# Kernel optimization log

Measured on AMD Instinct MI355X. Metric: run time of the kernel, lower is better.

## Reference

```python
import jax, jax.numpy as jnp
import numpy as np

N = 40000; E = 640000; F_IN = 128; HID = 32; HEADS = 4; G = 64
NEG_SLOPE = 0.2; LN_EPS = 1e-5


def setup_inputs() -> dict:
    key = jax.random.key(0)
    ks = jax.random.split(key, 24)
    rn = lambda k, shape, s=0.1: jax.random.normal(k, shape, jnp.float32) * s
    d = {}
    d["x"] = jax.random.normal(ks[0], (N, F_IN), jnp.float32)
    d["edge_index"] = jax.random.randint(ks[1], (2, E), 0, N)
    d["batch"] = jnp.sort(jax.random.randint(ks[2], (N,), 0, G))
    # GAT layer 0: in F_IN -> HID per head, HEADS heads, concat
    d["W0"] = rn(ks[3], (F_IN, HEADS * HID))
    d["as0"] = rn(ks[4], (HEADS, HID)); d["ad0"] = rn(ks[5], (HEADS, HID))
    d["b0"] = jnp.zeros((HEADS * HID,), jnp.float32)
    d["ln0_g"] = jnp.ones((HEADS * HID,), jnp.float32); d["ln0_b"] = jnp.zeros((HEADS * HID,), jnp.float32)
    # GAT layer 1: HEADS*HID -> HID per head, HEADS heads, concat
    d["W1"] = rn(ks[6], (HEADS * HID, HEADS * HID))
    d["as1"] = rn(ks[7], (HEADS, HID)); d["ad1"] = rn(ks[8], (HEADS, HID))
    d["b1"] = jnp.zeros((HEADS * HID,), jnp.float32)
    d["ln1_g"] = jnp.ones((HEADS * HID,), jnp.float32); d["ln1_b"] = jnp.zeros((HEADS * HID,), jnp.float32)
    # GAT layer 2: HEADS*HID -> HID, 1 head, no concat
    d["W2"] = rn(ks[9], (HEADS * HID, HID))
    d["as2"] = rn(ks[10], (1, HID)); d["ad2"] = rn(ks[11], (1, HID))
    d["b2"] = jnp.zeros((HID,), jnp.float32)
    d["ln2_g"] = jnp.ones((HID,), jnp.float32); d["ln2_b"] = jnp.zeros((HID,), jnp.float32)
    # classifier: HID -> HID//2 -> 2
    d["fc1_w"] = rn(ks[12], (HID, HID // 2)); d["fc1_b"] = jnp.zeros((HID // 2,), jnp.float32)
    d["fc2_w"] = rn(ks[13], (HID // 2, 2)); d["fc2_b"] = jnp.zeros((2,), jnp.float32)
    return d


def gat_layer(x, src, dst, W, a_s, a_d, b, heads, out_c, concat):
    n = x.shape[0]
    h = (x @ W).reshape(n, heads, out_c)            # [N,H,C]
    al_s = jnp.sum(h * a_s, axis=-1)                # [N,H]
    al_d = jnp.sum(h * a_d, axis=-1)                # [N,H]
    e = jax.nn.leaky_relu(al_s[src] + al_d[dst], NEG_SLOPE)  # [E,H]
    m = jax.ops.segment_max(e, dst, num_segments=n)          # segment softmax over dst
    ex = jnp.exp(e - m[dst])
    s = jax.ops.segment_sum(ex, dst, num_segments=n)
    alpha = ex / (s[dst] + 1e-16)                   # [E,H]
    out = jax.ops.segment_sum(h[src] * alpha[:, :, None], dst, num_segments=n)  # [N,H,C]
    out = out.reshape(n, heads * out_c) if concat else out.mean(axis=1)
    return out + b


def layer_norm(x, g, b):
    mu = x.mean(-1, keepdims=True)
    var = jnp.var(x, axis=-1, keepdims=True)
    return (x - mu) * jax.lax.rsqrt(var + LN_EPS) * g + b


def reference(x, edge_index, batch, W0, as0, ad0, b0, ln0_g, ln0_b, W1, as1, ad1, b1, ln1_g, ln1_b, W2, as2, ad2, b2, ln2_g, ln2_b, fc1_w, fc1_b, fc2_w, fc2_b):
    src, dst = edge_index[0], edge_index[1]
    h = gat_layer(x, src, dst, W0, as0, ad0, b0, HEADS, HID, True)
    h = jax.nn.elu(layer_norm(h, ln0_g, ln0_b))
    h = gat_layer(h, src, dst, W1, as1, ad1, b1, HEADS, HID, True)
    h = jax.nn.elu(layer_norm(h, ln1_g, ln1_b))
    h = gat_layer(h, src, dst, W2, as2, ad2, b2, 1, HID, False)
    h = jax.nn.elu(layer_norm(h, ln2_g, ln2_b))
    cnt = jax.ops.segment_sum(jnp.ones((h.shape[0],), h.dtype), batch, num_segments=G)
    hg = jax.ops.segment_sum(h, batch, num_segments=G) / jnp.maximum(cnt, 1.0)[:, None]  # global mean pool [G,HID]
    z = jax.nn.relu(hg @ fc1_w + fc1_b)
    return z @ fc2_w + fc2_b
```

## Files before the change

### kernel.cpp

```cpp
#include <hip/hip_runtime.h>
#include <hip/hip_fp16.h>
#include <math.h>

#define NN 40000
#define EE 640000
#define NG 64
#define SCAN_BLOCKS ((NN + 1023) / 1024)

__device__ __forceinline__ float eluf(float x) { return x > 0.f ? x : expm1f(x); }

typedef const __attribute__((address_space(1))) char gas_char;
typedef __attribute__((address_space(3))) char las_char;

__device__ __forceinline__ void async_copy16(void* l, const void* g) {
  __builtin_amdgcn_global_load_lds((gas_char*)g, (las_char*)l, 16, 0, 0);
}

typedef __fp16 f16x2 __attribute__((ext_vector_type(2)));
__device__ __forceinline__ unsigned packh(float lo, float hi) {
  f16x2 p = __builtin_amdgcn_cvt_pkrtz(lo, hi);
  union { f16x2 h; unsigned u; } c; c.h = p; return c.u;
}
__device__ __forceinline__ float hlo(unsigned p) {
  union { unsigned u; f16x2 h; } c; c.u = p; return (float)c.h.x;
}
__device__ __forceinline__ float hhi(unsigned p) {
  union { unsigned u; f16x2 h; } c; c.u = p; return (float)c.h.y;
}

__global__ void zero_int_kernel(int* __restrict__ p, int n) {
  int i = blockIdx.x * 256 + threadIdx.x;
  if (i < n) p[i] = 0;
}

__global__ void count_deg_kernel(const int* __restrict__ dst, int* __restrict__ deg, int e) {
  int i0 = (blockIdx.x * 256 + threadIdx.x) * 2;
  if (i0 + 2 <= e) {
    int2 d2 = *reinterpret_cast<const int2*>(&dst[i0]);
    atomicAdd(&deg[d2.x], 1);
    atomicAdd(&deg[d2.y], 1);
  } else {
    for (int i = i0; i < e; ++i) atomicAdd(&deg[dst[i]], 1);
  }
}

__global__ __launch_bounds__(1024) void scanA_kernel(const int* __restrict__ deg,
                                                     int* __restrict__ row_ptr,
                                                     int* __restrict__ bsum, int n) {
  __shared__ int wsum[16];
  int t = threadIdx.x, lane = t & 63, wid = t >> 6;
  int i = blockIdx.x * 1024 + t;
  int v = (i < n) ? deg[i] : 0;
#pragma unroll
  for (int off = 1; off < 64; off <<= 1) {
    int u = __shfl_up(v, off);
    if (lane >= off) v += u;
  }
  if (lane == 63) wsum[wid] = v;
  __syncthreads();
  if (t < 16) {
    int w = wsum[t];
#pragma unroll
    for (int off = 1; off < 16; off <<= 1) {
      int u = __shfl_up(w, off);
      if (t >= off) w += u;
    }
    wsum[t] = w;
  }
  __syncthreads();
  if (wid > 0) v += wsum[wid - 1];
  if (i < n) row_ptr[i + 1] = v;
  if (t == 1023) bsum[blockIdx.x] = v;
}

__global__ __launch_bounds__(1024) void scanC_kernel(int* __restrict__ row_ptr,
                                                     const int* __restrict__ bsum,
                                                     int* __restrict__ cursor, int n) {
  __shared__ int off_s;
  int t = threadIdx.x;
  int b = blockIdx.x;
  if (t < 64) {
    int v = (t < b && t < SCAN_BLOCKS) ? bsum[t] : 0;
#pragma unroll
    for (int m = 1; m < 64; m <<= 1) v += __shfl_xor(v, m);
    if (t == 0) off_s = v;
  }
  __syncthreads();
  int off = off_s;
  int i = b * 1024 + t;
  if (i < n) {
    int v = row_ptr[i + 1] + off;
    row_ptr[i + 1] = v;
    if (i + 1 < n) cursor[i + 1] = v;
    if (i == 0) { cursor[0] = 0; row_ptr[0] = 0; }
  }
}

__global__ void scatter_kernel(const int* __restrict__ src, const int* __restrict__ dst,
                               int* __restrict__ cursor, int* __restrict__ csr_src, int e) {
  int i0 = (blockIdx.x * 256 + threadIdx.x) * 2;
  if (i0 + 2 <= e) {
    int2 s2 = *reinterpret_cast<const int2*>(&src[i0]);
    int2 d2 = *reinterpret_cast<const int2*>(&dst[i0]);
    int p0 = atomicAdd(&cursor[d2.x], 1);
    int p1 = atomicAdd(&cursor[d2.y], 1);
    csr_src[p0] = s2.x;
    csr_src[p1] = s2.y;
  } else {
    for (int i = i0; i < e; ++i) {
      int d = dst[i];
      int pos = atomicAdd(&cursor[d], 1);
      csr_src[pos] = src[i];
    }
  }
}

__global__ __launch_bounds__(256, 3) void gemm128_kernel(
    const float* __restrict__ x, const float* __restrict__ W,
    const float* __restrict__ a_s, const float* __restrict__ a_d,
    unsigned* __restrict__ hb, float* __restrict__ als, float* __restrict__ ald)
{
  __shared__ float xs[2][64 * 32];
  __shared__ float ws[2][32 * 128];

  int t = threadIdx.x;
  int row0 = blockIdx.x * 64;
  const char* xgb = (const char*)x + (size_t)row0 * 512;

  {
    int li0 = t, li1 = t + 256;
    async_copy16((char*)xs[0] + li0 * 16, xgb + (li0 >> 3) * 512 + (li0 & 7) * 16);
    async_copy16((char*)xs[0] + li1 * 16, xgb + (li1 >> 3) * 512 + (li1 & 7) * 16);
    const char* wg = (const char*)W;
#pragma unroll
    for (int p = 0; p < 4; ++p)
      async_copy16((char*)ws[0] + p * 4096 + t * 16, wg + p * 4096 + t * 16);
  }
  __syncthreads();

  int cg = t & 31, rg = t >> 5;
  int r0 = rg * 8;
  int jlo = 2 * cg;

  float acc[8][4];
#pragma unroll
  for (int r = 0; r < 8; ++r)
#pragma unroll
    for (int c = 0; c < 4; ++c) acc[r][c] = 0.f;

  for (int ch = 0; ch < 4; ++ch) {
    if (ch < 3) {
      int b = (ch + 1) & 1;
      int li0 = t, li1 = t + 256;
      const char* xg = xgb + (ch + 1) * 128;
      async_copy16((char*)xs[b] + li0 * 16, xg + (li0 >> 3) * 512 + (li0 & 7) * 16);
      async_copy16((char*)xs[b] + li1 * 16, xg + (li1 >> 3) * 512 + (li1 & 7) * 16);
      const char* wg = (const char*)W + (size_t)(ch + 1) * 32 * 128 * 4;
#pragma unroll
      for (int p = 0; p < 4; ++p)
        async_copy16((char*)ws[b] + p * 4096 + t * 16, wg + p * 4096 + t * 16);
    }
    const float* wc = ws[ch & 1];
    const float* xc = xs[ch & 1];
#pragma unroll
    for (int kk = 0; kk < 32; kk += 4) {
      float2 wlo[4], whi[4];
#pragma unroll
      for (int q = 0; q < 4; ++q) {
        wlo[q] = *reinterpret_cast<const float2*>(&wc[(kk + q) * 128 + jlo]);
        whi[q] = *reinterpret_cast<const float2*>(&wc[(kk + q) * 128 + 64 + jlo]);
      }
#pragma unroll
      for (int r = 0; r < 8; ++r) {
        float4 xv = *reinterpret_cast<const float4*>(&xc[(r0 + r) * 32 + kk]);
        float a0 = acc[r][0], a1 = acc[r][1], a2 = acc[r][2], a3 = acc[r][3];
        a0 = fmaf(xv.x, wlo[0].x, a0); a1 = fmaf(xv.x, wlo[0].y, a1);
        a2 = fmaf(xv.x, whi[0].x, a2); a3 = fmaf(xv.x, whi[0].y, a3);
        a0 = fmaf(xv.y, wlo[1].x, a0); a1 = fmaf(xv.y, wlo[1].y, a1);
        a2 = fmaf(xv.y, whi[1].x, a2); a3 = fmaf(xv.y, whi[1].y, a3);
        a0 = fmaf(xv.z, wlo[2].x, a0); a1 = fmaf(xv.z, wlo[2].y, a1);
        a2 = fmaf(xv.z, whi[2].x, a2); a3 = fmaf(xv.z, whi[2].y, a3);
        a0 = fmaf(xv.w, wlo[3].x, a0); a1 = fmaf(xv.w, wlo[3].y, a1);
        a2 = fmaf(xv.w, whi[3].x, a2); a3 = fmaf(xv.w, whi[3].y, a3);
        acc[r][0] = a0; acc[r][1] = a1; acc[r][2] = a2; acc[r][3] = a3;
      }
    }
    __syncthreads();
  }

#pragma unroll
  for (int r = 0; r < 8; ++r) {
    uint2 pv;
    pv.x = packh(acc[r][0], acc[r][2]);
    pv.y = packh(acc[r][1], acc[r][3]);
    *reinterpret_cast<uint2*>(&hb[(size_t)(row0 + r0 + r) * 64 + jlo]) = pv;
  }

  float as0 = a_s[jlo], as1 = a_s[jlo + 1], as2 = a_s[jlo + 64], as3 = a_s[jlo + 65];
  float ad0 = a_d[jlo], ad1 = a_d[jlo + 1], ad2 = a_d[jlo + 64], ad3 = a_d[jlo + 65];
  int lane = t & 63;
#pragma unroll
  for (int r = 0; r < 8; ++r) {
    float psa = fmaf(acc[r][0], as0, acc[r][1] * as1);
    float psb = fmaf(acc[r][2], as2, acc[r][3] * as3);
    float pda = fmaf(acc[r][0], ad0, acc[r][1] * ad1);
    float pdb = fmaf(acc[r][2], ad2, acc[r][3] * ad3);
#pragma unroll
    for (int m = 1; m < 16; m <<= 1) {
      psa += __shfl_xor(psa, m); psb += __shfl_xor(psb, m);
      pda += __shfl_xor(pda, m); pdb += __shfl_xor(pdb, m);
    }
    if ((lane & 15) == 0) {
      int hA = (lane >> 4) & 1;
      size_t row = (size_t)(row0 + r0 + r);
      als[row * 4 + hA] = psa; als[row * 4 + hA + 2] = psb;
      ald[row * 4 + hA] = pda; ald[row * 4 + hA + 2] = pdb;
    }
  }
}

template<bool FUSE>
__global__ __launch_bounds__(256) void aggregate128_kernel(
    const unsigned* __restrict__ hb, const float* __restrict__ als, const float* __restrict__ ald,
    const int* __restrict__ row_ptr, const int* __restrict__ csr_src,
    const float* __restrict__ bias, const float* __restrict__ ln_g, const float* __restrict__ ln_b,
    float* __restrict__ out,
    const float* __restrict__ W2, const float* __restrict__ as2, const float* __restrict__ ad2,
    unsigned short* __restrict__ h2h, float* __restrict__ als2, float* __restrict__ ald2)
{
  __shared__ int s_src[4][4][17];
  __shared__ float2 s_w[4][4][17][2];
  __shared__ __align__(16) float w2s[FUSE ? 32 * 128 : 4];
  __shared__ __align__(16) float y_s[FUSE ? 16 * 132 : 4];

  int t = threadIdx.x, lane = t & 63, wid = t >> 6;
  int q = lane >> 4, c4 = lane & 15;
  int node = blockIdx.x * 16 + wid * 4 + q;

  if constexpr (FUSE) {
#pragma unroll
    for (int p = 0; p < 4; ++p)
      async_copy16((char*)w2s + p * 4096 + t * 16, (const char*)W2 + p * 4096 + t * 16);
    __syncthreads();
  }

  int start = row_ptr[node], end = row_ptr[node + 1];
  int deg = end - start;

  float4 adq = reinterpret_cast<const float4*>(ald)[node];
  int hsel = c4 >> 3;
  const uint4* hbase = reinterpret_cast<const uint4*>(hb + 4 * c4);
  float a0 = 0.f, a1 = 0.f, a2 = 0.f, a3 = 0.f;
  float a4 = 0.f, a5 = 0.f, a6 = 0.f, a7 = 0.f;
  float b0 = 0.f, b1 = 0.f, b2 = 0.f, b3 = 0.f;
  float b4 = 0.f, b5 = 0.f, b6 = 0.f, b7 = 0.f;
  float ssum0 = 0.f, ssum1 = 0.f, sb0 = 0.f, sb1 = 0.f;

  for (int eb = 0; eb < deg; eb += 16) {
    int s = 0;
    float ex0 = 0.f, ex1 = 0.f, ex2 = 0.f, ex3 = 0.f;
    if (eb + c4 < deg) {
      s = csr_src[start + eb + c4];
      float4 qv = reinterpret_cast<const float4*>(als)[s];
      float v0 = qv.x + adq.x, v1 = qv.y + adq.y, v2 = qv.z + adq.z, v3 = qv.w + adq.w;
      v0 = v0 > 0.f ? v0 : 0.2f * v0; v1 = v1 > 0.f ? v1 : 0.2f * v1;
      v2 = v2 > 0.f ? v2 : 0.2f * v2; v3 = v3 > 0.f ? v3 : 0.2f * v3;
      ex0 = __expf(v0); ex1 = __expf(v1); ex2 = __expf(v2); ex3 = __expf(v3);
    }
    s_src[wid][q][c4] = s;
    s_w[wid][q][c4][0] = make_float2(ex0, ex2);
    s_w[wid][q][c4][1] = make_float2(ex1, ex3);

    int cnt = deg - eb; if (cnt > 16) cnt = 16;
    int j = 0;
    for (; j + 2 <= cnt; j += 2) {
      int sa = s_src[wid][q][j];
      int sb = s_src[wid][q][j + 1];
      uint4 ua = hbase[(size_t)sa * 16];
      uint4 ub = hbase[(size_t)sb * 16];
      float2 wa = s_w[wid][q][j][hsel];
      float2 wb = s_w[wid][q][j + 1][hsel];
      a0 = fmaf(wa.x, hlo(ua.x), a0); a1 = fmaf(wa.x, hlo(ua.y), a1);
      a2 = fmaf(wa.x, hlo(ua.z), a2); a3 = fmaf(wa.x, hlo(ua.w), a3);
      a4 = fmaf(wa.y, hhi(ua.x), a4); a5 = fmaf(wa.y, hhi(ua.y), a5);
      a6 = fmaf(wa.y, hhi(ua.z), a6); a7 = fmaf(wa.y, hhi(ua.w), a7);
      ssum0 += wa.x; ssum1 += wa.y;
      b0 = fmaf(wb.x, hlo(ub.x), b0); b1 = fmaf(wb.x, hlo(ub.y), b1);
      b2 = fmaf(wb.x, hlo(ub.z), b2); b3 = fmaf(wb.x, hlo(ub.w), b3);
      b4 = fmaf(wb.y, hhi(ub.x), b4); b5 = fmaf(wb.y, hhi(ub.y), b5);
      b6 = fmaf(wb.y, hhi(ub.z), b6); b7 = fmaf(wb.y, hhi(ub.w), b7);
      sb0 += wb.x; sb1 += wb.y;
    }
    if (j < cnt) {
      int sa = s_src[wid][q][j];
      uint4 ua = hbase[(size_t)sa * 16];
      float2 wa = s_w[wid][q][j][hsel];
      a0 = fmaf(wa.x, hlo(ua.x), a0); a1 = fmaf(wa.x, hlo(ua.y), a1);
      a2 = fmaf(wa.x, hlo(ua.z), a2); a3 = fmaf(wa.x, hlo(ua.w), a3);
      a4 = fmaf(wa.y, hhi(ua.x), a4); a5 = fmaf(wa.y, hhi(ua.y), a5);
      a6 = fmaf(wa.y, hhi(ua.z), a6); a7 = fmaf(wa.y, hhi(ua.w), a7);
      ssum0 += wa.x; ssum1 += wa.y;
    }
  }
  a0 += b0; a1 += b1; a2 += b2; a3 += b3;
  a4 += b4; a5 += b5; a6 += b6; a7 += b7;
  ssum0 += sb0; ssum1 += sb1;

  float4 blo = *reinterpret_cast<const float4*>(&bias[4 * c4]);
  float4 bhi = *reinterpret_cast<const float4*>(&bias[64 + 4 * c4]);
  float is0 = 1.f / (ssum0 + 1e-16f), is1 = 1.f / (ssum1 + 1e-16f);
  float o0 = a0 * is0 + blo.x, o1 = a1 * is0 + blo.y;
  float o2 = a2 * is0 + blo.z, o3 = a3 * is0 + blo.w;
  float o4 = a4 * is1 + bhi.x, o5 = a5 * is1 + bhi.y;
  float o6 = a6 * is1 + bhi.z, o7 = a7 * is1 + bhi.w;
  float red = (o0 + o1 + o2 + o3) + (o4 + o5 + o6 + o7);
  float sq2 = (o0 * o0 + o1 * o1 + o2 * o2 + o3 * o3)
            + (o4 * o4 + o5 * o5 + o6 * o6 + o7 * o7);
#pragma unroll
  for (int m = 1; m < 16; m <<= 1) {
    red += __shfl_xor(red, m);
    sq2 += __shfl_xor(sq2, m);
  }
  float mu = red * (1.f / 128.f);
  float var = sq2 * (1.f / 128.f) - mu * mu;
  float rstd = rsqrtf(var + 1e-5f);
  float4 glo = *reinterpret_cast<const float4*>(&ln_g[4 * c4]);
  float4 ghi = *reinterpret_cast<const float4*>(&ln_g[64 + 4 * c4]);
  float4 bl2 = *reinterpret_cast<const float4*>(&ln_b[4 * c4]);
  float4 bh2 = *reinterpret_cast<const float4*>(&ln_b[64 + 4 * c4]);
  float4 ylo, yhi;
  ylo.x = eluf((o0 - mu) * rstd * glo.x + bl2.x);
  ylo.y = eluf((o1 - mu) * rstd * glo.y + bl2.y);
  ylo.z = eluf((o2 - mu) * rstd * glo.z + bl2.z);
  ylo.w = eluf((o3 - mu) * rstd * glo.w + bl2.w);
  yhi.x = eluf((o4 - mu) * rstd * ghi.x + bh2.x);
  yhi.y = eluf((o5 - mu) * rstd * ghi.y + bh2.y);
  yhi.z = eluf((o6 - mu) * rstd * ghi.z + bh2.z);
  yhi.w = eluf((o7 - mu) * rstd * ghi.w + bh2.w);

  if constexpr (!FUSE) {
    *reinterpret_cast<float4*>(&out[(size_t)node * 128 + 4 * c4]) = ylo;
    *reinterpret_cast<float4*>(&out[(size_t)node * 128 + 64 + 4 * c4]) = yhi;
  } else {
    int nidx = (wid * 4 + q) * 132;
    *reinterpret_cast<float4*>(&y_s[nidx + 4 * c4]) = ylo;
    *reinterpret_cast<float4*>(&y_s[nidx + 64 + 4 * c4]) = yhi;
    float d0 = 0.f, d1 = 0.f, d2 = 0.f, d3 = 0.f;
#pragma unroll
    for (int k = 0; k < 128; k += 2) {
      float2 yv = *reinterpret_cast<const float2*>(&y_s[nidx + k]);
      d0 = fmaf(yv.x, w2s[k * 32 + c4], d0);
      d1 = fmaf(yv.y, w2s[(k + 1) * 32 + c4], d1);
      d2 = fmaf(yv.x, w2s[k * 32 + c4 + 16], d2);
      d3 = fmaf(yv.y, w2s[(k + 1) * 32 + c4 + 16], d3);
    }
    float accA = d0 + d1, accB = d2 + d3;
    unsigned pa = packh(accA, accB);
    h2h[(size_t)node * 32 + c4] = (unsigned short)(pa & 0xffffu);
    h2h[(size_t)node * 32 + c4 + 16] = (unsigned short)(pa >> 16);
    float ps = fmaf(accA, as2[c4], accB * as2[c4 + 16]);
    float pd = fmaf(accA, ad2[c4], accB * ad2[c4 + 16]);
#pragma unroll
    for (int m = 1; m < 16; m <<= 1) { ps += __shfl_xor(ps, m); pd += __shfl_xor(pd, m); }
    if (c4 == 0) { als2[node] = ps; ald2[node] = pd; }
  }
}

__global__ __launch_bounds__(256) void aggregate32_kernel(
    const unsigned short* __restrict__ h, const float* __restrict__ als, const float* __restrict__ ald,
    const int* __restrict__ row_ptr, const int* __restrict__ csr_src,
    const float* __restrict__ bias, const float* __restrict__ ln_g, const float* __restrict__ ln_b,
    float* __restrict__ out, int n)
{
  __shared__ int s_src[4][4][17];
  __shared__ float s_ex[4][4][17];
  int t = threadIdx.x, lane = t & 63, wid = t >> 6;
  int q = lane >> 4, c4 = lane & 15;
  int node = blockIdx.x * 16 + wid * 4 + q;
  int start = row_ptr[node], end = row_ptr[node + 1];
  int deg = end - start;
  float adl = ald[node];
  const unsigned* hu = reinterpret_cast<const unsigned*>(h);
  float acc0 = 0.f, acc1 = 0.f, bc0 = 0.f, bc1 = 0.f;
  float ssum = 0.f, sb = 0.f;

  for (int eb = 0; eb < deg; eb += 16) {
    int s = 0; float ex = 0.f;
    if (eb + c4 < deg) {
      s = csr_src[start + eb + c4];
      float v = als[s] + adl;
      v = v > 0.f ? v : 0.2f * v;
      ex = __expf(v);
    }
    s_src[wid][q][c4] = s;
    s_ex[wid][q][c4] = ex;

    int cnt = deg - eb; if (cnt > 16) cnt = 16;
    int j = 0;
    for (; j + 2 <= cnt; j += 2) {
      int sa = s_src[wid][q][j];
      int sbx = s_src[wid][q][j + 1];
      unsigned ua = hu[(size_t)sa * 16 + c4];
      unsigned ub = hu[(size_t)sbx * 16 + c4];
      float wa = s_ex[wid][q][j];
      float wb = s_ex[wid][q][j + 1];
      acc0 = fmaf(wa, hlo(ua), acc0); acc1 = fmaf(wa, hhi(ua), acc1); ssum += wa;
      bc0 = fmaf(wb, hlo(ub), bc0); bc1 = fmaf(wb, hhi(ub), bc1); sb += wb;
    }
    if (j < cnt) {
      int sa = s_src[wid][q][j];
      unsigned ua = hu[(size_t)sa * 16 + c4];
      float wa = s_ex[wid][q][j];
      acc0 = fmaf(wa, hlo(ua), acc0); acc1 = fmaf(wa, hhi(ua), acc1); ssum += wa;
    }
  }
  acc0 += bc0; acc1 += bc1; ssum += sb;

  float2 bv = *reinterpret_cast<const float2*>(&bias[2 * c4]);
  float is = 1.f / (ssum + 1e-16f);
  float o0 = acc0 * is + bv.x;
  float o1 = acc1 * is + bv.y;
  float red = o0 + o1, sq2 = o0 * o0 + o1 * o1;
#pragma unroll
  for (int m = 1; m < 16; m <<= 1) {
    red += __shfl_xor(red, m);
    sq2 += __shfl_xor(sq2, m);
  }
  float mu = red * (1.f / 32.f);
  float var = sq2 * (1.f / 32.f) - mu * mu;
  float rstd = rsqrtf(var + 1e-5f);
  float2 gv = *reinterpret_cast<const float2*>(&ln_g[2 * c4]);
  float2 lb = *reinterpret_cast<const float2*>(&ln_b[2 * c4]);
  float2 yv;
  yv.x = eluf((o0 - mu) * rstd * gv.x + lb.x);
  yv.y = eluf((o1 - mu) * rstd * gv.y + lb.y);
  *reinterpret_cast<float2*>(&out[(size_t)node * 32 + 2 * c4]) = yv;
}

__device__ __forceinline__ int lower_bound_dev(const int* a, int n, int key) {
  int lo = 0, hi = n;
  while (lo < hi) { int mid = (lo + hi) >> 1; if (a[mid] < key) lo = mid + 1; else hi = mid; }
  return lo;
}

__global__ __launch_bounds__(256) void poolfc_kernel(
    const float* __restrict__ x2, const int* __restrict__ batch,
    const float* __restrict__ fc1w, const float* __restrict__ fc1b,
    const float* __restrict__ fc2w, const float* __restrict__ fc2b,
    float* __restrict__ out, int n)
{
  int g = blockIdx.x;
  int lo = lower_bound_dev(batch, n, g);
  int hi = lower_bound_dev(batch, n, g + 1);
  int t = threadIdx.x;
  int c = t & 31, r = t >> 5;
  float acc = 0.f;
  for (int i = lo + r; i < hi; i += 8) acc += x2[(size_t)i * 32 + c];
  __shared__ float red[8][32];
  __shared__ float hgl[32];
  __shared__ float zl[16];
  red[r][c] = acc;
  __syncthreads();
  if (r == 0) {
    float s = 0.f;
#pragma unroll
    for (int k = 0; k < 8; ++k) s += red[k][c];
    float cnt = (float)(hi - lo);
    hgl[c] = s / fmaxf(cnt, 1.f);
  }
  __syncthreads();
  if (t < 16) {
    float a = fc1b[t];
#pragma unroll
    for (int k = 0; k < 32; ++k) a = fmaf(hgl[k], fc1w[k * 16 + t], a);
    zl[t] = fmaxf(a, 0.f);
  }
  __syncthreads();
  if (t < 2) {
    float a = fc2b[t];
#pragma unroll
    for (int j = 0; j < 16; ++j) a = fmaf(zl[j], fc2w[j * 2 + t], a);
    out[g * 2 + t] = a;
  }
}

extern "C" void kernel_launch(void* const* d_in, const int* in_sizes, int n_in,
                              void* d_out, int out_size, void* d_ws, size_t ws_size,
                              hipStream_t stream) {
  const float* x    = (const float*)d_in[0];
  const int*   ei   = (const int*)d_in[1];
  const int*   batch= (const int*)d_in[2];
  const float* W0   = (const float*)d_in[3];
  const float* as0  = (const float*)d_in[4];
  const float* ad0  = (const float*)d_in[5];
  const float* b0   = (const float*)d_in[6];
  const float* ln0g = (const float*)d_in[7];
  const float* ln0b = (const float*)d_in[8];
  const float* W1   = (const float*)d_in[9];
  const float* as1  = (const float*)d_in[10];
  const float* ad1  = (const float*)d_in[11];
  const float* b1   = (const float*)d_in[12];
  const float* ln1g = (const float*)d_in[13];
  const float* ln1b = (const float*)d_in[14];
  const float* W2   = (const float*)d_in[15];
  const float* as2  = (const float*)d_in[16];
  const float* ad2  = (const float*)d_in[17];
  const float* b2   = (const float*)d_in[18];
  const float* ln2g = (const float*)d_in[19];
  const float* ln2b = (const float*)d_in[20];
  const float* fc1w = (const float*)d_in[21];
  const float* fc1b = (const float*)d_in[22];
  const float* fc2w = (const float*)d_in[23];
  const float* fc2b = (const float*)d_in[24];
  float* out = (float*)d_out;

  const int* srce = ei;
  const int* dste = ei + EE;

  unsigned* hb = (unsigned*)d_ws;
  float* B2  = (float*)(hb + (size_t)NN * 64);
  float* als = B2 + (size_t)NN * 128;
  float* ald = als + (size_t)NN * 4;
  unsigned short* h2h = (unsigned short*)(ald + (size_t)NN * 4);
  float* x2  = (float*)(h2h + (size_t)NN * 32);
  float* als2 = x2 + (size_t)NN * 32;
  float* ald2 = als2 + NN;
  int* deg      = (int*)(ald2 + NN);
  int* row_ptr  = deg + NN;
  int* cursor   = row_ptr + NN + 1;
  int* csr_src  = cursor + NN;
  int* bsum     = csr_src + EE;

  zero_int_kernel<<<(NN + 255) / 256, 256, 0, stream>>>(deg, NN);
  count_deg_kernel<<<(EE / 2 + 255) / 256, 256, 0, stream>>>(dste, deg, EE);
  scanA_kernel<<<SCAN_BLOCKS, 1024, 0, stream>>>(deg, row_ptr, bsum, NN);
  scanC_kernel<<<SCAN_BLOCKS, 1024, 0, stream>>>(row_ptr, bsum, cursor, NN);
  scatter_kernel<<<(EE / 2 + 255) / 256, 256, 0, stream>>>(srce, dste, cursor, csr_src, EE);

  gemm128_kernel<<<625, 256, 0, stream>>>(x, W0, as0, ad0, hb, als, ald);
  aggregate128_kernel<false><<<NN / 16, 256, 0, stream>>>(hb, als, ald, row_ptr, csr_src,
                                                          b0, ln0g, ln0b, B2,
                                                          nullptr, nullptr, nullptr,
                                                          nullptr, nullptr, nullptr);
  gemm128_kernel<<<625, 256, 0, stream>>>(B2, W1, as1, ad1, hb, als, ald);
  aggregate128_kernel<true><<<NN / 16, 256, 0, stream>>>(hb, als, ald, row_ptr, csr_src,
                                                         b1, ln1g, ln1b, nullptr,
                                                         W2, as2, ad2, h2h, als2, ald2);
  aggregate32_kernel<<<NN / 16, 256, 0, stream>>>(h2h, als2, ald2, row_ptr, csr_src,
                                                  b2, ln2g, ln2b, x2, NN);
  poolfc_kernel<<<NG, 256, 0, stream>>>(x2, batch, fc1w, fc1b, fc2w, fc2b, out, NN);
}
```

Baseline: 244.6 us.

## Fuse CSR scatter with layer-0 GEMM into one interleaved launch

Merges the edge scatter kernel and the first-layer GEMM into a single kernel of 1875 blocks. Every third block runs the GEMM tile and the other two each scatter a 512-edge chunk. The atomic-bound scatter and the compute-bound GEMM can then overlap on the GPU, and one launch and its boundary go away. In exchange, scatter blocks carry the GEMM's shared-memory allocation and launch bounds, which may cap how many blocks fit per CU.

```diff
diff --git a/kernel.cpp b/kernel.cpp
--- a/kernel.cpp
+++ b/kernel.cpp
@@ -96,21 +96,130 @@
   }
 }
 
-__global__ void scatter_kernel(const int* __restrict__ src, const int* __restrict__ dst,
-                               int* __restrict__ cursor, int* __restrict__ csr_src, int e) {
-  int i0 = (blockIdx.x * 256 + threadIdx.x) * 2;
-  if (i0 + 2 <= e) {
-    int2 s2 = *reinterpret_cast<const int2*>(&src[i0]);
-    int2 d2 = *reinterpret_cast<const int2*>(&dst[i0]);
-    int p0 = atomicAdd(&cursor[d2.x], 1);
-    int p1 = atomicAdd(&cursor[d2.y], 1);
-    csr_src[p0] = s2.x;
-    csr_src[p1] = s2.y;
-  } else {
-    for (int i = i0; i < e; ++i) {
-      int d = dst[i];
-      int pos = atomicAdd(&cursor[d], 1);
-      csr_src[pos] = src[i];
+__global__ __launch_bounds__(256, 3) void gemm_scatter_kernel(
+    const float* __restrict__ x, const float* __restrict__ W,
+    const float* __restrict__ a_s, const float* __restrict__ a_d,
+    unsigned* __restrict__ hb, float* __restrict__ als, float* __restrict__ ald,
+    const int* __restrict__ src, const int* __restrict__ dst,
+    int* __restrict__ cursor, int* __restrict__ csr_src, int e)
+{
+  __shared__ float xs[2][64 * 32];
+  __shared__ float ws[2][32 * 128];
+
+  int bx = blockIdx.x;
+  int t = threadIdx.x;
+
+  if (bx % 3 != 2) {
+    int sid = (bx / 3) * 2 + (bx % 3 == 1 ? 1 : 0);
+    int i0 = (sid * 256 + t) * 2;
+    if (i0 + 2 <= e) {
+      int2 s2 = *reinterpret_cast<const int2*>(&src[i0]);
+      int2 d2 = *reinterpret_cast<const int2*>(&dst[i0]);
+      int p0 = atomicAdd(&cursor[d2.x], 1);
+      int p1 = atomicAdd(&cursor[d2.y], 1);
+      csr_src[p0] = s2.x;
+      csr_src[p1] = s2.y;
+    } else {
+      for (int i = i0; i < e; ++i) {
+        int d = dst[i];
+        int pos = atomicAdd(&cursor[d], 1);
+        csr_src[pos] = src[i];
+      }
+    }
+    return;
+  }
+
+  int row0 = (bx / 3) * 64;
+  const char* xgb = (const char*)x + (size_t)row0 * 512;
+
+  {
+    int li0 = t, li1 = t + 256;
+    async_copy16((char*)xs[0] + li0 * 16, xgb + (li0 >> 3) * 512 + (li0 & 7) * 16);
+    async_copy16((char*)xs[0] + li1 * 16, xgb + (li1 >> 3) * 512 + (li1 & 7) * 16);
+    const char* wg = (const char*)W;
+#pragma unroll
+    for (int p = 0; p < 4; ++p)
+      async_copy16((char*)ws[0] + p * 4096 + t * 16, wg + p * 4096 + t * 16);
+  }
+  __syncthreads();
+
+  int cg = t & 31, rg = t >> 5;
+  int r0 = rg * 8;
+  int jlo = 2 * cg;
+
+  float acc[8][4];
+#pragma unroll
+  for (int r = 0; r < 8; ++r)
+#pragma unroll
+    for (int c = 0; c < 4; ++c) acc[r][c] = 0.f;
+
+  for (int ch = 0; ch < 4; ++ch) {
+    if (ch < 3) {
+      int b = (ch + 1) & 1;
+      int li0 = t, li1 = t + 256;
+      const char* xg = xgb + (ch + 1) * 128;
+      async_copy16((char*)xs[b] + li0 * 16, xg + (li0 >> 3) * 512 + (li0 & 7) * 16);
+      async_copy16((char*)xs[b] + li1 * 16, xg + (li1 >> 3) * 512 + (li1 & 7) * 16);
+      const char* wg = (const char*)W + (size_t)(ch + 1) * 32 * 128 * 4;
+#pragma unroll
+      for (int p = 0; p < 4; ++p)
+        async_copy16((char*)ws[b] + p * 4096 + t * 16, wg + p * 4096 + t * 16);
+    }
+    const float* wc = ws[ch & 1];
+    const float* xc = xs[ch & 1];
+#pragma unroll
+    for (int kk = 0; kk < 32; kk += 4) {
+      float2 wlo[4], whi[4];
+#pragma unroll
+      for (int q = 0; q < 4; ++q) {
+        wlo[q] = *reinterpret_cast<const float2*>(&wc[(kk + q) * 128 + jlo]);
+        whi[q] = *reinterpret_cast<const float2*>(&wc[(kk + q) * 128 + 64 + jlo]);
+      }
+#pragma unroll
+      for (int r = 0; r < 8; ++r) {
+        float4 xv = *reinterpret_cast<const float4*>(&xc[(r0 + r) * 32 + kk]);
+        float a0 = acc[r][0], a1 = acc[r][1], a2 = acc[r][2], a3 = acc[r][3];
+        a0 = fmaf(xv.x, wlo[0].x, a0); a1 = fmaf(xv.x, wlo[0].y, a1);
+        a2 = fmaf(xv.x, whi[0].x, a2); a3 = fmaf(xv.x, whi[0].y, a3);
+        a0 = fmaf(xv.y, wlo[1].x, a0); a1 = fmaf(xv.y, wlo[1].y, a1);
+        a2 = fmaf(xv.y, whi[1].x, a2); a3 = fmaf(xv.y, whi[1].y, a3);
+        a0 = fmaf(xv.z, wlo[2].x, a0); a1 = fmaf(xv.z, wlo[2].y, a1);
+        a2 = fmaf(xv.z, whi[2].x, a2); a3 = fmaf(xv.z, whi[2].y, a3);
+        a0 = fmaf(xv.w, wlo[3].x, a0); a1 = fmaf(xv.w, wlo[3].y, a1);
+        a2 = fmaf(xv.w, whi[3].x, a2); a3 = fmaf(xv.w, whi[3].y, a3);
+        acc[r][0] = a0; acc[r][1] = a1; acc[r][2] = a2; acc[r][3] = a3;
+      }
+    }
+    __syncthreads();
+  }
+
+#pragma unroll
+  for (int r = 0; r < 8; ++r) {
+    uint2 pv;
+    pv.x = packh(acc[r][0], acc[r][2]);
+    pv.y = packh(acc[r][1], acc[r][3]);
+    *reinterpret_cast<uint2*>(&hb[(size_t)(row0 + r0 + r) * 64 + jlo]) = pv;
+  }
+
+  float as0 = a_s[jlo], as1 = a_s[jlo + 1], as2 = a_s[jlo + 64], as3 = a_s[jlo + 65];
+  float ad0 = a_d[jlo], ad1 = a_d[jlo + 1], ad2 = a_d[jlo + 64], ad3 = a_d[jlo + 65];
+  int lane = t & 63;
+#pragma unroll
+  for (int r = 0; r < 8; ++r) {
+    float psa = fmaf(acc[r][0], as0, acc[r][1] * as1);
+    float psb = fmaf(acc[r][2], as2, acc[r][3] * as3);
+    float pda = fmaf(acc[r][0], ad0, acc[r][1] * ad1);
+    float pdb = fmaf(acc[r][2], ad2, acc[r][3] * ad3);
+#pragma unroll
+    for (int m = 1; m < 16; m <<= 1) {
+      psa += __shfl_xor(psa, m); psb += __shfl_xor(psb, m);
+      pda += __shfl_xor(pda, m); pdb += __shfl_xor(pdb, m);
+    }
+    if ((lane & 15) == 0) {
+      int hA = (lane >> 4) & 1;
+      size_t row = (size_t)(row0 + r0 + r);
+      als[row * 4 + hA] = psa; als[row * 4 + hA + 2] = psb;
+      ald[row * 4 + hA] = pda; ald[row * 4 + hA + 2] = pdb;
     }
   }
 }
@@ -535,9 +644,10 @@
   count_deg_kernel<<<(EE / 2 + 255) / 256, 256, 0, stream>>>(dste, deg, EE);
   scanA_kernel<<<SCAN_BLOCKS, 1024, 0, stream>>>(deg, row_ptr, bsum, NN);
   scanC_kernel<<<SCAN_BLOCKS, 1024, 0, stream>>>(row_ptr, bsum, cursor, NN);
-  scatter_kernel<<<(EE / 2 + 255) / 256, 256, 0, stream>>>(srce, dste, cursor, csr_src, EE);
-
-  gemm128_kernel<<<625, 256, 0, stream>>>(x, W0, as0, ad0, hb, als, ald);
+
+  gemm_scatter_kernel<<<1875, 256, 0, stream>>>(x, W0, as0, ad0, hb, als, ald,
+                                                srce, dste, cursor, csr_src, EE);
+
   aggregate128_kernel<false><<<NN / 16, 256, 0, stream>>>(hb, als, ald, row_ptr, csr_src,
                                                           b0, ln0g, ln0b, B2,
                                                           nullptr, nullptr, nullptr,
```

New measurement: 231.9 us. 5.2% less time.
